# Performance work log

Measured on AMD Instinct MI355X. Metric: run time of the kernel, lower is better.

The kernel has to match this reference:

```python
import jax, jax.numpy as jnp
import numpy as np

B, A, D, K = 262144, 10, 10, 32  # batch, aspects, aspect dim (=10), projection dim


def setup_inputs() -> dict:
    key = jax.random.key(0)
    ks = jax.random.split(key, 7)
    scale = 0.01
    return {
        "user_rep": jax.random.normal(ks[0], (B, A, D), jnp.float32),
        "item_rep": jax.random.normal(ks[1], (B, A, D), jnp.float32),
        "affinity_matrix": jax.random.uniform(ks[2], (D, D), jnp.float32, -scale, scale),
        "user_projection": jax.random.uniform(ks[3], (K, D), jnp.float32, -scale, scale),
        "user_parameters": jax.random.uniform(ks[4], (K, 1), jnp.float32, -scale, scale),
        "item_projection": jax.random.uniform(ks[5], (K, D), jnp.float32, -scale, scale),
        "item_parameters": jax.random.uniform(ks[6], (K, 1), jnp.float32, -scale, scale),
    }


def reference(user_rep, item_rep, affinity_matrix, user_projection,
              user_parameters, item_projection, item_parameters):
    # affinity: relu( U @ M @ V^T )  -> [B, Au, Av]
    aff = jax.nn.relu(jnp.einsum('bud,de,bve->buv', user_rep, affinity_matrix, item_rep))

    h_user = jnp.einsum('kd,bud->bku', user_projection, user_rep)  # [B,K,Au]
    h_item = jnp.einsum('kd,bvd->bkv', item_projection, item_rep)  # [B,K,Av]

    # user importance branch
    hu = jax.nn.relu(h_user + jnp.einsum('bkv,buv->bku', h_item, aff))
    u_score = jnp.einsum('k,bku->bu', user_parameters[:, 0], hu)   # [B,Au]
    user_asp_importance = jax.nn.softmax(u_score, axis=1)

    # item importance branch
    hi = jax.nn.relu(h_item + jnp.einsum('bku,buv->bkv', h_user, aff))
    i_score = jnp.einsum('k,bkv->bv', item_parameters[:, 0], hi)   # [B,Av]
    item_asp_importance = jax.nn.softmax(i_score, axis=1)

    return (user_asp_importance, item_asp_importance)
```

## Files before the change

### kernel.cpp

```cpp
#include <hip/hip_runtime.h>

#define NB 262144
#define AA 10
#define DD 10
#define KK 32

typedef unsigned int uint32;
typedef _Float16 h2 __attribute__((ext_vector_type(2)));

#if defined(__has_builtin)
#if __has_builtin(__builtin_amdgcn_fdot2)
#define HAVE_FDOT2 1
#endif
#endif

#ifdef HAVE_FDOT2
static __device__ __forceinline__ float fdot2(h2 a, h2 b, float c) {
    return __builtin_amdgcn_fdot2(a, b, c, false);
}
#else
static __device__ __forceinline__ float fdot2(h2 a, h2 b, float c) {
    return fmaf((float)a.x, (float)b.x, fmaf((float)a.y, (float)b.y, c));
}
#endif

static __device__ __forceinline__ h2 pkrtz(float lo, float hi) {
    auto r = __builtin_amdgcn_cvt_pkrtz(lo, hi);
    union { decltype(r) a; h2 h; } c; c.a = r; return c.h;
}
static __device__ __forceinline__ h2 u2h(uint32 u) {
    union { uint32 u; h2 h; } c; c.u = u; return c.h;
}
static __device__ __forceinline__ uint32 h2u(h2 h) {
    union { uint32 u; h2 h; } c; c.h = h; return c.u;
}
static __device__ __forceinline__ h2 dup_lo(h2 x) { return __builtin_shufflevector(x, x, 0, 0); }
static __device__ __forceinline__ h2 dup_hi(h2 x) { return __builtin_shufflevector(x, x, 1, 1); }

static __device__ __forceinline__ float b2f(unsigned short h) {
    union { uint32 u; float f; } c; c.u = ((uint32)h) << 16; return c.f;
}
static __device__ __forceinline__ float bflo(uint32 w) {
    union { uint32 u; float f; } c; c.u = w << 16; return c.f;
}
static __device__ __forceinline__ float bfhi(uint32 w) {
    union { uint32 u; float f; } c; c.u = w & 0xffff0000u; return c.f;
}

__device__ __forceinline__ int detect_f32(const unsigned short* p, int nshorts,
                                          unsigned expthr, int lane) {
    int bad = 0;
    if (lane < nshorts) {
        unsigned e = (p[lane] >> 7) & 0xFFu;
        bad = (e >= expthr);
    }
    return __any(bad);
}

__global__ __launch_bounds__(64) void prep_weights(
    const unsigned short* __restrict__ wM,
    const unsigned short* __restrict__ wPu,
    const unsigned short* __restrict__ wpu,
    const unsigned short* __restrict__ wPi,
    const unsigned short* __restrict__ wpi,
    uint32* __restrict__ wf)
{
    const int t = threadIdx.x;
    int f = 0;
    f |= detect_f32(wM,  64, 125, t) << 0;
    f |= detect_f32(wPu, 64, 125, t) << 1;
    f |= detect_f32(wpu, 32, 125, t) << 2;
    f |= detect_f32(wPi, 64, 125, t) << 3;
    f |= detect_f32(wpi, 32, 125, t) << 4;
    const float* fM  = (const float*)wM;
    const float* fPu = (const float*)wPu;
    const float* fpu = (const float*)wpu;
    const float* fPi = (const float*)wPi;
    const float* fpi = (const float*)wpi;

    for (int i = t; i < 50; i += 64) {
        const int d = i / 5, j = i % 5;
        float a = (f & 1) ? fM[d * 10 + 2 * j]     : b2f(wM[d * 10 + 2 * j]);
        float c = (f & 1) ? fM[d * 10 + 2 * j + 1] : b2f(wM[d * 10 + 2 * j + 1]);
        wf[i] = h2u(pkrtz(a, c));
    }
    for (int n = t; n < KK * 12; n += 64) {
        const int k = n / 12, j = n % 12;
        uint32 vu = 0, vi = 0;
        if (j < 5) {
            float a0 = (f & 2) ? fPu[k * 10 + 2 * j]     : b2f(wPu[k * 10 + 2 * j]);
            float a1 = (f & 2) ? fPu[k * 10 + 2 * j + 1] : b2f(wPu[k * 10 + 2 * j + 1]);
            float b0 = (f & 8) ? fPi[k * 10 + 2 * j]     : b2f(wPi[k * 10 + 2 * j]);
            float b1 = (f & 8) ? fPi[k * 10 + 2 * j + 1] : b2f(wPi[k * 10 + 2 * j + 1]);
            vu = h2u(pkrtz(a0, a1));
            vi = h2u(pkrtz(b0, b1));
        } else if (j < 10) {
            const int jj = j - 5;
            float a0 = (f & 8) ? fPi[k * 10 + 2 * jj]     : b2f(wPi[k * 10 + 2 * jj]);
            float a1 = (f & 8) ? fPi[k * 10 + 2 * jj + 1] : b2f(wPi[k * 10 + 2 * jj + 1]);
            float b0 = (f & 2) ? fPu[k * 10 + 2 * jj]     : b2f(wPu[k * 10 + 2 * jj]);
            float b1 = (f & 2) ? fPu[k * 10 + 2 * jj + 1] : b2f(wPu[k * 10 + 2 * jj + 1]);
            vu = h2u(pkrtz(a0, a1));
            vi = h2u(pkrtz(b0, b1));
        } else if (j == 10) {
            float a = (f & 4)  ? fpu[k] : b2f(wpu[k]);
            float b = (f & 16) ? fpi[k] : b2f(wpi[k]);
            union { float f; uint32 u; } ca, cb; ca.f = a; cb.f = b;
            vu = ca.u; vi = cb.u;
        }
        wf[64 + n]  = vu;
        wf[576 + n] = vi;
    }
}

static __device__ __forceinline__ void load_rep_h(const unsigned short* __restrict__ p,
                                                  int isf32, long long b, h2 R[AA][5]) {
    if (!isf32) {
        const uint2* g = (const uint2*)(p + b * 100);
        #pragma unroll
        for (int j = 0; j < 25; j++) {
            uint2 w = g[j];
            int e = 2 * j;
            R[e / 5][e % 5]             = pkrtz(bflo(w.x), bfhi(w.x));
            R[(e + 1) / 5][(e + 1) % 5] = pkrtz(bflo(w.y), bfhi(w.y));
        }
    } else {
        const float4* g = (const float4*)((const float*)p + b * 100);
        #pragma unroll
        for (int j = 0; j < 25; j++) {
            float4 w = g[j];
            int e = 2 * j;
            R[e / 5][e % 5]             = pkrtz(w.x, w.y);
            R[(e + 1) / 5][(e + 1) % 5] = pkrtz(w.z, w.w);
        }
    }
}

__global__ __launch_bounds__(64, 3) void aie_main(
    const unsigned short* __restrict__ user_rep,
    const unsigned short* __restrict__ item_rep,
    const uint32* __restrict__ wf,
    float* __restrict__ out)
{
    const int t = threadIdx.x;
    const long long b = (long long)blockIdx.x * 64 + t;
    const float* wff = (const float*)wf;

    const int fu = detect_f32(user_rep, 64, 137, t);
    const int fi = detect_f32(item_rep, 64, 137, t);

    h2 Uh[AA][5], Vh[AA][5];
    load_rep_h(item_rep, fi, b, Vh);
    load_rep_h(user_rep, fu, b, Uh);

    float us[AA];
    #pragma unroll
    for (int u = 0; u < AA; u++) {
        h2 um[5];
        {
            h2 d0 = dup_lo(Uh[u][0]);
            #pragma unroll
            for (int j = 0; j < 5; j++) um[j] = d0 * u2h(wf[j]);
        }
        #pragma unroll
        for (int d = 1; d < DD; d++) {
            h2 dd = (d & 1) ? dup_hi(Uh[u][d >> 1]) : dup_lo(Uh[u][d >> 1]);
            #pragma unroll
            for (int j = 0; j < 5; j++) um[j] += dd * u2h(wf[d * 5 + j]);
        }
        h2 Wr[5];
        #pragma unroll
        for (int j = 0; j < 5; j++) Wr[j] = pkrtz(0.f, 0.f);
        #pragma unroll
        for (int v = 0; v < AA; v++) {
            float r = 0.f;
            #pragma unroll
            for (int j = 0; j < 5; j++) r = fdot2(um[j], Vh[v][j], r);
            r = fmaxf(r, 0.f);
            h2 rd = pkrtz(r, r);
            #pragma unroll
            for (int j = 0; j < 5; j++) Wr[j] += rd * Vh[v][j];
        }
        float acc = 0.f;
        #pragma unroll 2
        for (int k = 0; k < KK; k++) {
            const int o = 64 + 12 * k;
            float s = 0.f;
            #pragma unroll
            for (int j = 0; j < 5; j++) s = fdot2(u2h(wf[o + j]), Uh[u][j], s);
            #pragma unroll
            for (int j = 0; j < 5; j++) s = fdot2(u2h(wf[o + 5 + j]), Wr[j], s);
            acc += wff[o + 10] * fmaxf(s, 0.f);
        }
        us[u] = acc;
    }

    {
        float mx = us[0];
        #pragma unroll
        for (int u = 1; u < AA; u++) mx = fmaxf(mx, us[u]);
        float s = 0.f;
        #pragma unroll
        for (int u = 0; u < AA; u++) { us[u] = __expf(us[u] - mx); s += us[u]; }
        const float inv = 1.f / s;
        float* o0 = out + b * 10;
        #pragma unroll
        for (int j = 0; j < 5; j++)
            *(float2*)(o0 + 2 * j) = make_float2(us[2 * j] * inv, us[2 * j + 1] * inv);
    }

    float isc[AA];
    #pragma unroll
    for (int v = 0; v < AA; v++) {
        float mvf[DD];
        #pragma unroll
        for (int d = 0; d < DD; d++) {
            float x = 0.f;
            #pragma unroll
            for (int j = 0; j < 5; j++) x = fdot2(u2h(wf[d * 5 + j]), Vh[v][j], x);
            mvf[d] = x;
        }
        h2 mv[5];
        #pragma unroll
        for (int j = 0; j < 5; j++) mv[j] = pkrtz(mvf[2 * j], mvf[2 * j + 1]);

        h2 Xr[5];
        #pragma unroll
        for (int j = 0; j < 5; j++) Xr[j] = pkrtz(0.f, 0.f);
        #pragma unroll
        for (int u = 0; u < AA; u++) {
            float r = 0.f;
            #pragma unroll
            for (int j = 0; j < 5; j++) r = fdot2(mv[j], Uh[u][j], r);
            r = fmaxf(r, 0.f);
            h2 rd = pkrtz(r, r);
            #pragma unroll
            for (int j = 0; j < 5; j++) Xr[j] += rd * Uh[u][j];
        }
        float acc = 0.f;
        #pragma unroll 2
        for (int k = 0; k < KK; k++) {
            const int o = 576 + 12 * k;
            float s = 0.f;
            #pragma unroll
            for (int j = 0; j < 5; j++) s = fdot2(u2h(wf[o + j]), Vh[v][j], s);
            #pragma unroll
            for (int j = 0; j < 5; j++) s = fdot2(u2h(wf[o + 5 + j]), Xr[j], s);
            acc += wff[o + 10] * fmaxf(s, 0.f);
        }
        isc[v] = acc;
    }

    {
        float mx = isc[0];
        #pragma unroll
        for (int v = 1; v < AA; v++) mx = fmaxf(mx, isc[v]);
        float s = 0.f;
        #pragma unroll
        for (int v = 0; v < AA; v++) { isc[v] = __expf(isc[v] - mx); s += isc[v]; }
        const float inv = 1.f / s;
        float* o1 = out + (size_t)NB * 10 + b * 10;
        #pragma unroll
        for (int j = 0; j < 5; j++)
            *(float2*)(o1 + 2 * j) = make_float2(isc[2 * j] * inv, isc[2 * j + 1] * inv);
    }
}

extern "C" void kernel_launch(void* const* d_in, const int* in_sizes, int n_in,
                              void* d_out, int out_size, void* d_ws, size_t ws_size,
                              hipStream_t stream) {
    const unsigned short* user_rep = (const unsigned short*)d_in[0];
    const unsigned short* item_rep = (const unsigned short*)d_in[1];
    uint32* wf = (uint32*)d_ws;

    hipLaunchKernelGGL(prep_weights, dim3(1), dim3(64), 0, stream,
                       (const unsigned short*)d_in[2], (const unsigned short*)d_in[3],
                       (const unsigned short*)d_in[4], (const unsigned short*)d_in[5],
                       (const unsigned short*)d_in[6], wf);

    hipLaunchKernelGGL(aie_main, dim3(NB / 64), dim3(64), 0, stream,
                       user_rep, item_rep, wf, (float*)d_out);
}
```

Measured before the change: 320.9 us.

## Split user and item branches into separate blocks with streamed rows

Launches twice as many blocks, with each block computing only the user or the item importance branch. Each thread holds one representation in registers and streams the other one aspect row at a time. Scores are staged in shared memory so the aspect loop can stay rolled, and a transposed copy of the affinity matrix is prepared for the item side. The aim is lower register pressure and higher occupancy (launch bounds raised from 3 to 5), at the cost of reading each input twice and recomputing the projections in both blocks.

```diff
diff --git a/kernel.cpp b/kernel.cpp
--- a/kernel.cpp
+++ b/kernel.cpp
@@ -34,8 +34,6 @@
 static __device__ __forceinline__ uint32 h2u(h2 h) {
     union { uint32 u; h2 h; } c; c.h = h; return c.u;
 }
-static __device__ __forceinline__ h2 dup_lo(h2 x) { return __builtin_shufflevector(x, x, 0, 0); }
-static __device__ __forceinline__ h2 dup_hi(h2 x) { return __builtin_shufflevector(x, x, 1, 1); }
 
 static __device__ __forceinline__ float b2f(unsigned short h) {
     union { uint32 u; float f; } c; c.u = ((uint32)h) << 16; return c.f;
@@ -78,11 +76,18 @@
     const float* fPi = (const float*)wPi;
     const float* fpi = (const float*)wpi;
 
-    for (int i = t; i < 50; i += 64) {
-        const int d = i / 5, j = i % 5;
-        float a = (f & 1) ? fM[d * 10 + 2 * j]     : b2f(wM[d * 10 + 2 * j]);
-        float c = (f & 1) ? fM[d * 10 + 2 * j + 1] : b2f(wM[d * 10 + 2 * j + 1]);
-        wf[i] = h2u(pkrtz(a, c));
+    for (int i = t; i < 100; i += 64) {
+        if (i < 50) {
+            const int d = i / 5, j = i % 5;
+            float a = (f & 1) ? fM[d * 10 + 2 * j]     : b2f(wM[d * 10 + 2 * j]);
+            float c = (f & 1) ? fM[d * 10 + 2 * j + 1] : b2f(wM[d * 10 + 2 * j + 1]);
+            wf[i] = h2u(pkrtz(a, c));
+        } else {
+            const int ii = i - 50, e = ii / 5, j = ii % 5;
+            float a = (f & 1) ? fM[(2 * j) * 10 + e]     : b2f(wM[(2 * j) * 10 + e]);
+            float c = (f & 1) ? fM[(2 * j + 1) * 10 + e] : b2f(wM[(2 * j + 1) * 10 + e]);
+            wf[i] = h2u(pkrtz(a, c));
+        }
     }
     for (int n = t; n < KK * 12; n += 64) {
         const int k = n / 12, j = n % 12;
@@ -108,8 +113,8 @@
             union { float f; uint32 u; } ca, cb; ca.f = a; cb.f = b;
             vu = ca.u; vi = cb.u;
         }
-        wf[64 + n]  = vu;
-        wf[576 + n] = vi;
+        wf[128 + n] = vu;
+        wf[512 + n] = vi;
     }
 }
 
@@ -136,133 +141,98 @@
     }
 }
 
-__global__ __launch_bounds__(64, 3) void aie_main(
+__global__ __launch_bounds__(64, 5) void aie_main(
     const unsigned short* __restrict__ user_rep,
     const unsigned short* __restrict__ item_rep,
     const uint32* __restrict__ wf,
     float* __restrict__ out)
 {
+    __shared__ float sc[64 * 11];
     const int t = threadIdx.x;
-    const long long b = (long long)blockIdx.x * 64 + t;
+    const int isItem = (int)(blockIdx.x >> 12);
+    const long long b = (long long)(blockIdx.x & 4095) * 64 + t;
+
+    const unsigned short* bulk = isItem ? user_rep : item_rep;
+    const unsigned short* strm = isItem ? item_rep : user_rep;
+    const int moff = isItem ? 0 : 50;
+    const int koff = isItem ? 512 : 128;
+
+    const int fb = detect_f32(bulk, 64, 137, t);
+    const int fs = detect_f32(strm, 64, 137, t);
+
+    h2 R[AA][5];
+    load_rep_h(bulk, fb, b, R);
+
     const float* wff = (const float*)wf;
 
-    const int fu = detect_f32(user_rep, 64, 137, t);
-    const int fi = detect_f32(item_rep, 64, 137, t);
-
-    h2 Uh[AA][5], Vh[AA][5];
-    load_rep_h(item_rep, fi, b, Vh);
-    load_rep_h(user_rep, fu, b, Uh);
-
-    float us[AA];
-    #pragma unroll
-    for (int u = 0; u < AA; u++) {
-        h2 um[5];
-        {
-            h2 d0 = dup_lo(Uh[u][0]);
-            #pragma unroll
-            for (int j = 0; j < 5; j++) um[j] = d0 * u2h(wf[j]);
-        }
-        #pragma unroll
-        for (int d = 1; d < DD; d++) {
-            h2 dd = (d & 1) ? dup_hi(Uh[u][d >> 1]) : dup_lo(Uh[u][d >> 1]);
-            #pragma unroll
-            for (int j = 0; j < 5; j++) um[j] += dd * u2h(wf[d * 5 + j]);
-        }
-        h2 Wr[5];
-        #pragma unroll
-        for (int j = 0; j < 5; j++) Wr[j] = pkrtz(0.f, 0.f);
-        #pragma unroll
-        for (int v = 0; v < AA; v++) {
+    #pragma unroll 1
+    for (int i = 0; i < AA; i++) {
+        h2 S[5];
+        if (!fs) {
+            const uint32* g = (const uint32*)(strm + b * 100 + (long long)i * 10);
+            #pragma unroll
+            for (int j = 0; j < 5; j++) { uint32 w = g[j]; S[j] = pkrtz(bflo(w), bfhi(w)); }
+        } else {
+            const float2* g = (const float2*)((const float*)strm + b * 100 + (long long)i * 10);
+            #pragma unroll
+            for (int j = 0; j < 5; j++) { float2 w = g[j]; S[j] = pkrtz(w.x, w.y); }
+        }
+
+        h2 T[5];
+        #pragma unroll
+        for (int x = 0; x < 5; x++) {
+            float t0 = 0.f, t1 = 0.f;
+            #pragma unroll
+            for (int j = 0; j < 5; j++) {
+                t0 = fdot2(u2h(wf[moff + (2 * x) * 5 + j]),     S[j], t0);
+                t1 = fdot2(u2h(wf[moff + (2 * x + 1) * 5 + j]), S[j], t1);
+            }
+            T[x] = pkrtz(t0, t1);
+        }
+
+        h2 A[5];
+        #pragma unroll
+        for (int j = 0; j < 5; j++) A[j] = pkrtz(0.f, 0.f);
+        #pragma unroll
+        for (int q = 0; q < AA; q++) {
             float r = 0.f;
             #pragma unroll
-            for (int j = 0; j < 5; j++) r = fdot2(um[j], Vh[v][j], r);
+            for (int j = 0; j < 5; j++) r = fdot2(T[j], R[q][j], r);
             r = fmaxf(r, 0.f);
             h2 rd = pkrtz(r, r);
             #pragma unroll
-            for (int j = 0; j < 5; j++) Wr[j] += rd * Vh[v][j];
-        }
+            for (int j = 0; j < 5; j++) A[j] += rd * R[q][j];
+        }
+
         float acc = 0.f;
         #pragma unroll 2
         for (int k = 0; k < KK; k++) {
-            const int o = 64 + 12 * k;
+            const int o = koff + 12 * k;
             float s = 0.f;
             #pragma unroll
-            for (int j = 0; j < 5; j++) s = fdot2(u2h(wf[o + j]), Uh[u][j], s);
-            #pragma unroll
-            for (int j = 0; j < 5; j++) s = fdot2(u2h(wf[o + 5 + j]), Wr[j], s);
+            for (int j = 0; j < 5; j++) s = fdot2(u2h(wf[o + j]), S[j], s);
+            #pragma unroll
+            for (int j = 0; j < 5; j++) s = fdot2(u2h(wf[o + 5 + j]), A[j], s);
             acc += wff[o + 10] * fmaxf(s, 0.f);
         }
-        us[u] = acc;
+        sc[t * 11 + i] = acc;
     }
 
     {
-        float mx = us[0];
-        #pragma unroll
-        for (int u = 1; u < AA; u++) mx = fmaxf(mx, us[u]);
+        float v[AA];
+        #pragma unroll
+        for (int i = 0; i < AA; i++) v[i] = sc[t * 11 + i];
+        float mx = v[0];
+        #pragma unroll
+        for (int i = 1; i < AA; i++) mx = fmaxf(mx, v[i]);
         float s = 0.f;
         #pragma unroll
-        for (int u = 0; u < AA; u++) { us[u] = __expf(us[u] - mx); s += us[u]; }
+        for (int i = 0; i < AA; i++) { v[i] = __expf(v[i] - mx); s += v[i]; }
         const float inv = 1.f / s;
-        float* o0 = out + b * 10;
+        float* o0 = out + (size_t)isItem * ((size_t)NB * 10) + b * 10;
         #pragma unroll
         for (int j = 0; j < 5; j++)
-            *(float2*)(o0 + 2 * j) = make_float2(us[2 * j] * inv, us[2 * j + 1] * inv);
-    }
-
-    float isc[AA];
-    #pragma unroll
-    for (int v = 0; v < AA; v++) {
-        float mvf[DD];
-        #pragma unroll
-        for (int d = 0; d < DD; d++) {
-            float x = 0.f;
-            #pragma unroll
-            for (int j = 0; j < 5; j++) x = fdot2(u2h(wf[d * 5 + j]), Vh[v][j], x);
-            mvf[d] = x;
-        }
-        h2 mv[5];
-        #pragma unroll
-        for (int j = 0; j < 5; j++) mv[j] = pkrtz(mvf[2 * j], mvf[2 * j + 1]);
-
-        h2 Xr[5];
-        #pragma unroll
-        for (int j = 0; j < 5; j++) Xr[j] = pkrtz(0.f, 0.f);
-        #pragma unroll
-        for (int u = 0; u < AA; u++) {
-            float r = 0.f;
-            #pragma unroll
-            for (int j = 0; j < 5; j++) r = fdot2(mv[j], Uh[u][j], r);
-            r = fmaxf(r, 0.f);
-            h2 rd = pkrtz(r, r);
-            #pragma unroll
-            for (int j = 0; j < 5; j++) Xr[j] += rd * Uh[u][j];
-        }
-        float acc = 0.f;
-        #pragma unroll 2
-        for (int k = 0; k < KK; k++) {
-            const int o = 576 + 12 * k;
-            float s = 0.f;
-            #pragma unroll
-            for (int j = 0; j < 5; j++) s = fdot2(u2h(wf[o + j]), Vh[v][j], s);
-            #pragma unroll
-            for (int j = 0; j < 5; j++) s = fdot2(u2h(wf[o + 5 + j]), Xr[j], s);
-            acc += wff[o + 10] * fmaxf(s, 0.f);
-        }
-        isc[v] = acc;
-    }
-
-    {
-        float mx = isc[0];
-        #pragma unroll
-        for (int v = 1; v < AA; v++) mx = fmaxf(mx, isc[v]);
-        float s = 0.f;
-        #pragma unroll
-        for (int v = 0; v < AA; v++) { isc[v] = __expf(isc[v] - mx); s += isc[v]; }
-        const float inv = 1.f / s;
-        float* o1 = out + (size_t)NB * 10 + b * 10;
-        #pragma unroll
-        for (int j = 0; j < 5; j++)
-            *(float2*)(o1 + 2 * j) = make_float2(isc[2 * j] * inv, isc[2 * j + 1] * inv);
+            *(float2*)(o0 + 2 * j) = make_float2(v[2 * j] * inv, v[2 * j + 1] * inv);
     }
 }
 
@@ -278,6 +248,6 @@
                        (const unsigned short*)d_in[4], (const unsigned short*)d_in[5],
                        (const unsigned short*)d_in[6], wf);
 
-    hipLaunchKernelGGL(aie_main, dim3(NB / 64), dim3(64), 0, stream,
+    hipLaunchKernelGGL(aie_main, dim3(2 * (NB / 64)), dim3(64), 0, stream,
                        user_rep, item_rep, wf, (float*)d_out);
 }
```

After: 340.9 us. 6.2% more time.
